# Optimization experiments

Hardware: AMD Instinct MI355X
Metric: run time of the kernel (lower is better)

The kernel has to match this reference:

```python
import jax, jax.numpy as jnp
import numpy as np

# model dims (match init_kwargs)
EMBED_DIM = 1024
NUM_HEADS = 16
HEAD_DIM = EMBED_DIM // NUM_HEADS  # 64
WS = 256           # window_size[0]*window_size[1] = 16*16
NW = 64            # number of windows
M = NW * WS        # gathered length = 16384
L = M - 1          # raw tokens (padding row appended makes M rows)
SCALE = HEAD_DIM ** -0.5


def _rope(t, cos, sin):
    # t: [M, H, d]; cos/sin: [M, d] -> broadcast over heads
    c = cos[:, None, :]
    s = sin[:, None, :]
    half = HEAD_DIM // 2
    rot = jnp.concatenate([-t[..., half:], t[..., :half]], axis=-1)
    return t * c + rot * s


def setup_inputs() -> dict:
    key = jax.random.key(0)
    ks = jax.random.split(key, 8)
    x = jax.random.normal(ks[0], (L, EMBED_DIM), jnp.float32)
    # kv_indices: permutation of all M rows (incl. padding row index L) so every
    # token lands in exactly one window slot, as the scatter-back assumes.
    kv_indices = jax.random.permutation(ks[1], M).astype(jnp.int64)
    q_indices = kv_indices            # unused in the manual (non-xformers) branch
    inv_indices = jnp.arange(L, dtype=jnp.int64)  # unused in the manual branch
    # rotary tables over gathered positions
    pos = jnp.arange(M, dtype=jnp.float32)
    inv_freq = 1.0 / (10000.0 ** (jnp.arange(0, HEAD_DIM, 2, dtype=jnp.float32) / HEAD_DIM))
    ang = pos[:, None] * inv_freq[None, :]          # [M, d/2]
    ang = jnp.concatenate([ang, ang], axis=-1)      # [M, d]
    rope_cos = jnp.cos(ang)
    rope_sin = jnp.sin(ang)
    # learned params
    qkv_w = jax.random.normal(ks[2], (3 * EMBED_DIM, EMBED_DIM), jnp.float32) * (EMBED_DIM ** -0.5)
    qkv_b = jax.random.normal(ks[3], (3 * EMBED_DIM,), jnp.float32) * 0.02
    proj_w = jax.random.normal(ks[4], (EMBED_DIM, EMBED_DIM), jnp.float32) * (EMBED_DIM ** -0.5)
    proj_b = jax.random.normal(ks[5], (EMBED_DIM,), jnp.float32) * 0.02
    padding = jnp.zeros((1, EMBED_DIM), jnp.float32)  # nn.Parameter(torch.zeros(1, D))
    return {"x": x, "qkv_w": qkv_w, "qkv_b": qkv_b, "proj_w": proj_w,
            "proj_b": proj_b, "padding": padding, "rope_cos": rope_cos,
            "rope_sin": rope_sin, "kv_indices": kv_indices,
            "q_indices": q_indices, "inv_indices": inv_indices, "ws": WS}


def reference(x, qkv_w, qkv_b, proj_w, proj_b, padding, rope_cos, rope_sin,
              kv_indices, q_indices, inv_indices, ws):
    # append padding row: [L+1, D]
    xp = jnp.concatenate([x, padding], axis=0)
    # fused qkv projection -> [M, 3, H, d]
    qkv = (xp @ qkv_w.T + qkv_b).reshape(-1, 3, NUM_HEADS, HEAD_DIM)
    q, k, v = qkv[:, 0], qkv[:, 1], qkv[:, 2]
    # manual windowed branch: gather q/k/v with kv_indices, RoPE (mode='key') on q and k
    qg = _rope(q[kv_indices], rope_cos, rope_sin)   # [M, H, d]
    kg = _rope(k[kv_indices], rope_cos, rope_sin)
    vg = v[kv_indices]
    nw = M // ws
    qw = qg.reshape(nw, ws, NUM_HEADS, HEAD_DIM)
    kw = kg.reshape(nw, ws, NUM_HEADS, HEAD_DIM)
    vw = vg.reshape(nw, ws, NUM_HEADS, HEAD_DIM)
    attn = jax.nn.softmax(SCALE * jnp.einsum('wind,wjnd->wnij', qw, kw), axis=-1)
    ow = jnp.einsum('wnij,wjnd->wind', attn, vw).reshape(M, NUM_HEADS * HEAD_DIM)
    # scatter back to original token order, drop padding row
    ori = jnp.zeros((M, EMBED_DIM), x.dtype).at[kv_indices].set(ow)
    out = ori[:L] @ proj_w.T + proj_b
    return out
```

## Files before the change

kernel.cpp:

```cpp
#include <hip/hip_runtime.h>
#include <hip/hip_bf16.h>

#define EMBED 1024
#define THREE_EMBED 3072
#define NHEAD 16
#define HDIM 64
#define MTOT 16384
#define LTOT 16383

typedef __attribute__((ext_vector_type(8))) short bf16x8;
typedef __attribute__((ext_vector_type(4))) float f32x4;

__device__ __forceinline__ unsigned short f2b(float f) {
  union { float f; unsigned u; } v; v.f = f;
  unsigned r = v.u + 0x7fffu + ((v.u >> 16) & 1u);
  return (unsigned short)(r >> 16);
}
__device__ __forceinline__ float b2f(unsigned short h) {
  union { unsigned u; float f; } v; v.u = ((unsigned)h) << 16;
  return v.f;
}

__device__ __forceinline__ void gload16(const void* g, void* l) {
  __builtin_amdgcn_global_load_lds(
      (const __attribute__((address_space(1))) void*)g,
      (__attribute__((address_space(3))) void*)l, 16, 0, 0);
}

#define BARRIER() asm volatile("s_barrier" ::: "memory")

__global__ __launch_bounds__(256) void cast_inputs(
    const float* __restrict__ x, const float* __restrict__ padding,
    const float* __restrict__ wq, const float* __restrict__ wp,
    const int* __restrict__ kvi,
    unsigned short* __restrict__ xb, unsigned short* __restrict__ wqb,
    unsigned short* __restrict__ wpb, int* __restrict__ inv, int np)
{
  const int NX = MTOT * EMBED / 8;
  const int NQ = THREE_EMBED * EMBED / 8;
  const int total = NX + NQ + np;
  int g = blockIdx.x * 256 + threadIdx.x;
  const int stride = gridDim.x * 256;
  for (; g < total + MTOT; g += stride) {
    if (g >= total) {
      int i = g - total;
      inv[kvi[i]] = i;
      continue;
    }
    const float* src;
    unsigned short* dst;
    if (g < NX) {
      size_t e = (size_t)g * 8;
      int row = (int)(e >> 10);
      src = (row < LTOT) ? (x + e) : (padding + (e - (size_t)LTOT * 1024));
      dst = xb + e;
    } else if (g < NX + NQ) {
      size_t e = (size_t)(g - NX) * 8;
      src = wq + e;
      dst = wqb + e;
    } else {
      size_t e = (size_t)(g - NX - NQ) * 8;
      src = wp + e;
      dst = wpb + e;
    }
    float4 a = *(const float4*)src;
    float4 b = *(const float4*)(src + 4);
    ushort4 u0, u1;
    u0.x = f2b(a.x); u0.y = f2b(a.y); u0.z = f2b(a.z); u0.w = f2b(a.w);
    u1.x = f2b(b.x); u1.y = f2b(b.y); u1.z = f2b(b.z); u1.w = f2b(b.w);
    *(ushort4*)dst = u0;
    *(ushort4*)(dst + 4) = u1;
  }
}

template <int EPI>
__global__ __launch_bounds__(512, 2) void gemm256(
    const unsigned short* __restrict__ A, const unsigned short* __restrict__ B,
    const float* __restrict__ bias, const int* __restrict__ idx,
    unsigned short* __restrict__ outb, float* __restrict__ outf)
{
  __shared__ __align__(16) unsigned short lds[65536];
  const int t = threadIdx.x;
  const int lane = t & 63, wid = t >> 6;
  const int l15 = lane & 15, quad = lane >> 4;
  const int wr = wid >> 2, wc = wid & 3;
  const int bm = blockIdx.x, bn = blockIdx.y;

  const int srow = wid * 8 + (lane >> 3);
  const int scol = ((lane & 7) ^ (lane >> 3)) * 8;
  const unsigned short* gA = A + (size_t)(bm * 256 + srow) * EMBED + scol;
  const unsigned short* gB = B + (size_t)(bn * 256 + srow) * EMBED + scol;

  auto stA = [&](int p, int R0, int kt) {
    const unsigned short* g = gA + (size_t)R0 * EMBED + kt * 64;
    char* d = (char*)lds + p * 32768 + R0 * 128 + wid * 1024;
    gload16(g, d);
    gload16(g + (size_t)64 * EMBED, d + 8192);
  };
  auto stB = [&](int p, int R0, int kt) {
    const unsigned short* g = gB + (size_t)R0 * EMBED + kt * 64;
    char* d = (char*)lds + 65536 + p * 32768 + R0 * 128 + wid * 1024;
    gload16(g, d);
    gload16(g + (size_t)64 * EMBED, d + 8192);
  };

  const int aOff = (wr * 128 + l15) * 64;
  const int bOff = (wc * 64 + l15) * 64;
  const int swz0 = (quad ^ (l15 & 7)) * 8;
  const int swz1 = ((quad + 4) ^ (l15 & 7)) * 8;

  f32x4 acc[8][4];
#pragma unroll
  for (int i = 0; i < 8; ++i)
#pragma unroll
    for (int j = 0; j < 4; ++j) acc[i][j] = (f32x4){0.f, 0.f, 0.f, 0.f};

  stA(0, 0, 0); stA(0, 128, 0); stB(0, 0, 0); stB(0, 128, 0);
  stB(1, 0, 1); stB(1, 128, 1);
  asm volatile("s_waitcnt vmcnt(4)" ::: "memory");
  BARRIER();

#define MFMAGRP(MB)                                                          \
  _Pragma("unroll") for (int m = 0; m < 4; ++m)                              \
      _Pragma("unroll") for (int n = 0; n < 4; ++n)                          \
          acc[(MB) + m][n] = __builtin_amdgcn_mfma_f32_16x16x32_bf16(        \
              a[m], b[n], acc[(MB) + m][n], 0, 0, 0);

#define TILE(P, KT, STA, STB, WCNT)                                          \
  {                                                                          \
    const unsigned short* Ab = lds + (P) * 16384 + aOff;                     \
    const unsigned short* Bb = lds + 32768 + (P) * 16384 + bOff;             \
    bf16x8 a[4], b[4];                                                       \
    {                                               \
      _Pragma("unroll") for (int n = 0; n < 4; ++n)                          \
          b[n] = *(const bf16x8*)(Bb + n * 1024 + swz0);                     \
      _Pragma("unroll") for (int m = 0; m < 4; ++m)                          \
          a[m] = *(const bf16x8*)(Ab + m * 1024 + swz0);                     \
      if (STA) stA((P) ^ 1, 0, (KT) + 1);                                    \
      BARRIER();                                                             \
      __builtin_amdgcn_s_setprio(1);                                         \
      MFMAGRP(0);                                                            \
      __builtin_amdgcn_s_setprio(0);                                         \
      BARRIER();                                                             \
    }                                                                        \
    {                                               \
      _Pragma("unroll") for (int m = 0; m < 4; ++m)                          \
          a[m] = *(const bf16x8*)(Ab + (4 + m) * 1024 + swz0);               \
      if (STA) stA((P) ^ 1, 128, (KT) + 1);                                  \
      BARRIER();                                                             \
      __builtin_amdgcn_s_setprio(1);                                         \
      MFMAGRP(4);                                                            \
      __builtin_amdgcn_s_setprio(0);                                         \
      BARRIER();                                                             \
    }                                                                        \
    {                                               \
      _Pragma("unroll") for (int n = 0; n < 4; ++n)                          \
          b[n] = *(const bf16x8*)(Bb + n * 1024 + swz1);                     \
      _Pragma("unroll") for (int m = 0; m < 4; ++m)                          \
          a[m] = *(const bf16x8*)(Ab + m * 1024 + swz1);                     \
      if (STB) stB((P), 0, (KT) + 2);                                        \
      BARRIER();                                                             \
      __builtin_amdgcn_s_setprio(1);                                         \
      MFMAGRP(0);                                                            \
      __builtin_amdgcn_s_setprio(0);                                         \
      BARRIER();                                                             \
    }                                                                        \
    {                                               \
      _Pragma("unroll") for (int m = 0; m < 4; ++m)                          \
          a[m] = *(const bf16x8*)(Ab + (4 + m) * 1024 + swz1);               \
      if (STB) stB((P), 128, (KT) + 2);                                      \
      BARRIER();                                                             \
      __builtin_amdgcn_s_setprio(1);                                         \
      MFMAGRP(4);                                                            \
      __builtin_amdgcn_s_setprio(0);                                         \
      if ((WCNT) == 4) asm volatile("s_waitcnt vmcnt(4)" ::: "memory");      \
      if ((WCNT) == 0) asm volatile("s_waitcnt vmcnt(0)" ::: "memory");      \
      BARRIER();                                                             \
    }                                                                        \
  }

#pragma unroll 1
  for (int t2 = 0; t2 < 7; ++t2) {
    const int kt = t2 * 2;
    TILE(0, kt, 1, 1, 4);
    TILE(1, kt + 1, 1, 1, 4);
  }
  TILE(0, 14, 1, 0, 0);
  TILE(1, 15, 0, 0, -1);
#undef TILE
#undef MFMAGRP

  float bv[4];
#pragma unroll
  for (int nt = 0; nt < 4; ++nt)
    bv[nt] = bias[bn * 256 + wc * 64 + nt * 16 + l15];
  if constexpr (EPI == 0) {
    const int hh = bn * 4 + wc;
    unsigned short* buf = outb + (size_t)hh * (MTOT * HDIM);
#pragma unroll
    for (int mt = 0; mt < 8; ++mt) {
#pragma unroll
      for (int reg = 0; reg < 4; ++reg) {
        int row = bm * 256 + wr * 128 + mt * 16 + quad * 4 + reg;
        int i = idx[row];
#pragma unroll
        for (int nt = 0; nt < 4; ++nt)
          buf[(size_t)i * HDIM + nt * 16 + l15] =
              f2b(acc[mt][nt][reg] + bv[nt]);
      }
    }
  } else {
    const int col = bn * 256 + wc * 64;
#pragma unroll
    for (int mt = 0; mt < 8; ++mt) {
#pragma unroll
      for (int reg = 0; reg < 4; ++reg) {
        int i = bm * 256 + wr * 128 + mt * 16 + quad * 4 + reg;
        int orow = idx[i];
        if (orow < LTOT) {
#pragma unroll
          for (int nt = 0; nt < 4; ++nt)
            outf[(size_t)orow * EMBED + col + nt * 16 + l15] =
                acc[mt][nt][reg] + bv[nt];
        }
      }
    }
  }
}

__global__ __launch_bounds__(256) void rope_qk(
    const float* __restrict__ rope_cos, const float* __restrict__ rope_sin,
    unsigned short* __restrict__ qkvh)
{
  int g = blockIdx.x * 256 + threadIdx.x;
  int dc = g & 3;
  int i  = (g >> 2) & (MTOT - 1);
  int hh = g >> 16;
  unsigned short* p = qkvh + ((size_t)hh * MTOT + i) * HDIM;
  bf16x8 lo = *(const bf16x8*)(p + dc * 8);
  bf16x8 hi = *(const bf16x8*)(p + 32 + dc * 8);
  const float* cp = rope_cos + (size_t)i * HDIM + dc * 8;
  const float* sp = rope_sin + (size_t)i * HDIM + dc * 8;
  float cl[8], ch[8], sl[8], sh[8];
  *(float4*)(cl)     = *(const float4*)(cp);
  *(float4*)(cl + 4) = *(const float4*)(cp + 4);
  *(float4*)(ch)     = *(const float4*)(cp + 32);
  *(float4*)(ch + 4) = *(const float4*)(cp + 36);
  *(float4*)(sl)     = *(const float4*)(sp);
  *(float4*)(sl + 4) = *(const float4*)(sp + 4);
  *(float4*)(sh)     = *(const float4*)(sp + 32);
  *(float4*)(sh + 4) = *(const float4*)(sp + 36);
  const float sc = (hh < 16) ? 0.125f : 1.0f;
  bf16x8 olo, ohi;
#pragma unroll
  for (int j = 0; j < 8; ++j) {
    float a = b2f((unsigned short)lo[j]);
    float b = b2f((unsigned short)hi[j]);
    olo[j] = (short)f2b((a * cl[j] - b * sl[j]) * sc);
    ohi[j] = (short)f2b((b * ch[j] + a * sh[j]) * sc);
  }
  *(bf16x8*)(p + dc * 8) = olo;
  *(bf16x8*)(p + 32 + dc * 8) = ohi;
}

__global__ __launch_bounds__(256) void cast_w(
    const float* __restrict__ w, unsigned short* __restrict__ wb)
{
  int g = blockIdx.x * 256 + threadIdx.x;
  size_t e = (size_t)g * 8;
  float4 a = *(const float4*)(w + e);
  float4 b = *(const float4*)(w + e + 4);
  ushort4 u0, u1;
  u0.x = f2b(a.x); u0.y = f2b(a.y); u0.z = f2b(a.z); u0.w = f2b(a.w);
  u1.x = f2b(b.x); u1.y = f2b(b.y); u1.z = f2b(b.z); u1.w = f2b(b.w);
  *(ushort4*)(wb + e) = u0;
  *(ushort4*)(wb + e + 4) = u1;
}

__global__ __launch_bounds__(256, 2) void attn(
    const unsigned short* __restrict__ qkvh,
    unsigned short* __restrict__ ow)
{
  __shared__ __align__(16) unsigned short sK[2][128 * 64];
  __shared__ __align__(16) unsigned short sV[2][64 * 128];
  __shared__ __align__(16) unsigned short sP[4][16 * 40];

  const int t = threadIdx.x;
  const int lane = t & 63, wid = t >> 6;
  const int l15 = lane & 15, quad = lane >> 4;
  const int wwin = blockIdx.x >> 4;
  const int h = blockIdx.x & 15;

  const unsigned short* Qh = qkvh + (size_t)h * (MTOT * HDIM);
  const unsigned short* Kh = qkvh + (size_t)(16 + h) * (MTOT * HDIM);
  const unsigned short* Vh = qkvh + (size_t)(32 + h) * (MTOT * HDIM);

  const int l3 = lane >> 3, l7 = lane & 7;
  const unsigned short* ksrc =
      Kh + (size_t)(wwin * 256 + wid * 32 + l3) * HDIM + (l7 ^ l3) * 8;
  auto stageK = [&](int buf, int half) {
#pragma unroll
    for (int p = 0; p < 4; ++p)
      gload16(ksrc + (size_t)(half * 128 + p * 8) * HDIM,
              (char*)&sK[buf][(wid * 32 + p * 8) * 64]);
  };

  const int vkey = t >> 1, vhx = t & 1;
  const unsigned short* vsrc =
      Vh + (size_t)(wwin * 256 + vkey) * HDIM + vhx * 32;
  auto writeV = [&](int buf, bf16x8* vr) {
    int kc3 = vkey >> 3, k7 = vkey & 7;
#pragma unroll
    for (int c = 0; c < 4; ++c)
#pragma unroll
      for (int j = 0; j < 8; ++j) {
        int d = vhx * 32 + c * 8 + j;
        sV[buf][d * 128 + ((kc3 ^ (d & 7)) * 8) + k7] =
            (unsigned short)vr[c][j];
      }
  };

  f32x4 accO[4][4];
  float mrow[4][4], lrow[4][4];
#pragma unroll
  for (int qt = 0; qt < 4; ++qt) {
#pragma unroll
    for (int nt = 0; nt < 4; ++nt) accO[qt][nt] = (f32x4){0.f, 0.f, 0.f, 0.f};
#pragma unroll
    for (int reg = 0; reg < 4; ++reg) { mrow[qt][reg] = -1e30f; lrow[qt][reg] = 0.f; }
  }

  stageK(0, 0);
  bf16x8 vr0[4], vr1[4];
#pragma unroll
  for (int c = 0; c < 4; ++c) vr0[c] = *(const bf16x8*)(vsrc + c * 8);
  bf16x8 qa[4][2];
#pragma unroll
  for (int qt = 0; qt < 4; ++qt) {
    int i = wwin * 256 + wid * 64 + qt * 16 + l15;
    const unsigned short* qp = Qh + (size_t)i * HDIM;
    qa[qt][0] = *(const bf16x8*)(qp + quad * 8);
    qa[qt][1] = *(const bf16x8*)(qp + 32 + quad * 8);
  }
  asm volatile("s_waitcnt vmcnt(0)" ::: "memory");
  writeV(0, vr0);
  stageK(1, 1);
#pragma unroll
  for (int c = 0; c < 4; ++c)
    vr1[c] = *(const bf16x8*)(vsrc + (size_t)128 * HDIM + c * 8);
  __syncthreads();

  auto compute = [&](const unsigned short* sKb, const unsigned short* sVb) {
#pragma unroll
    for (int qt = 0; qt < 4; ++qt) {
      f32x4 accS[8];
#pragma unroll
      for (int nt = 0; nt < 8; ++nt) accS[nt] = (f32x4){0.f, 0.f, 0.f, 0.f};
#pragma unroll
      for (int ks = 0; ks < 2; ++ks) {
#pragma unroll
        for (int nt = 0; nt < 8; ++nt) {
          int key = nt * 16 + l15;
          bf16x8 bk = *(const bf16x8*)(
              sKb + key * 64 + (((ks * 4 + quad) ^ (key & 7)) * 8));
          accS[nt] = __builtin_amdgcn_mfma_f32_16x16x32_bf16(
              qa[qt][ks], bk, accS[nt], 0, 0, 0);
        }
      }
#pragma unroll
      for (int reg = 0; reg < 4; ++reg) {
        float mx = accS[0][reg];
#pragma unroll
        for (int nt = 1; nt < 8; ++nt) mx = fmaxf(mx, accS[nt][reg]);
#pragma unroll
        for (int off = 1; off < 16; off <<= 1)
          mx = fmaxf(mx, __shfl_xor(mx, off, 64));
        float mold = mrow[qt][reg];
        float mnew = fmaxf(mold, mx);
        float alpha = __expf(mold - mnew);
        mrow[qt][reg] = mnew;
        float ls = 0.f;
#pragma unroll
        for (int nt = 0; nt < 8; ++nt) {
          float p = __expf(accS[nt][reg] - mnew);
          accS[nt][reg] = p;
          ls += p;
        }
#pragma unroll
        for (int off = 1; off < 16; off <<= 1) ls += __shfl_xor(ls, off, 64);
        lrow[qt][reg] = lrow[qt][reg] * alpha + ls;
#pragma unroll
        for (int nt = 0; nt < 4; ++nt) accO[qt][nt][reg] *= alpha;
      }
#pragma unroll
      for (int kc = 0; kc < 4; ++kc) {
#pragma unroll
        for (int nt2 = 0; nt2 < 2; ++nt2) {
#pragma unroll
          for (int reg = 0; reg < 4; ++reg) {
            sP[wid][(quad * 4 + reg) * 40 + nt2 * 16 + l15] =
                f2b(accS[kc * 2 + nt2][reg]);
          }
        }
        bf16x8 pa = *(const bf16x8*)(&sP[wid][l15 * 40 + quad * 8]);
#pragma unroll
        for (int nt = 0; nt < 4; ++nt) {
          int d = nt * 16 + l15;
          bf16x8 bv = *(const bf16x8*)(
              sVb + d * 128 + (((kc * 4 + quad) ^ (d & 7)) * 8));
          accO[qt][nt] = __builtin_amdgcn_mfma_f32_16x16x32_bf16(
              pa, bv, accO[qt][nt], 0, 0, 0);
        }
      }
    }
  };

  compute(&sK[0][0], &sV[0][0]);
  asm volatile("s_waitcnt vmcnt(0)" ::: "memory");
  __syncthreads();
  writeV(1, vr1);
  __syncthreads();
  compute(&sK[1][0], &sV[1][0]);

  __syncthreads();
  unsigned short* scr = &sK[0][0] + wid * 2048;
  const int rlane = lane >> 3;
  const int clane = (lane & 7) * 8;
#pragma unroll
  for (int qt = 0; qt < 4; ++qt) {
#pragma unroll
    for (int reg = 0; reg < 4; ++reg) {
      float invl = 1.0f / lrow[qt][reg];
      int r = quad * 4 + reg;
#pragma unroll
      for (int nt = 0; nt < 4; ++nt)
        scr[r * 72 + nt * 16 + l15] = f2b(accO[qt][nt][reg] * invl);
    }
#pragma unroll
    for (int rr = 0; rr < 2; ++rr) {
      int row = rr * 8 + rlane;
      bf16x8 vv = *(const bf16x8*)(scr + row * 72 + clane);
      int i = wwin * 256 + wid * 64 + qt * 16 + row;
      *(bf16x8*)(ow + (size_t)i * EMBED + h * HDIM + clane) = vv;
    }
  }
}

extern "C" void kernel_launch(void* const* d_in, const int* in_sizes, int n_in,
                              void* d_out, int out_size, void* d_ws, size_t ws_size,
                              hipStream_t stream) {
  const float* x        = (const float*)d_in[0];
  const float* qkv_w    = (const float*)d_in[1];
  const float* qkv_b    = (const float*)d_in[2];
  const float* proj_w   = (const float*)d_in[3];
  const float* proj_b   = (const float*)d_in[4];
  const float* padding  = (const float*)d_in[5];
  const float* rope_cos = (const float*)d_in[6];
  const float* rope_sin = (const float*)d_in[7];
  const int*   kvi      = (const int*)d_in[8];

  const size_t QKVH_B = (size_t)MTOT * THREE_EMBED * 2;
  const size_t R_B    = (size_t)MTOT * EMBED * 2;
  const size_t W_B    = (size_t)EMBED * EMBED * 2;
  unsigned short* qkvh = (unsigned short*)d_ws;
  unsigned short* R    = (unsigned short*)((char*)d_ws + QKVH_B);
  unsigned short* xb = R;
  unsigned short* ow = R;
  unsigned short* wqb = (unsigned short*)d_out;
  const bool roomy = ws_size >= QKVH_B + R_B + W_B;
  unsigned short* wpb = roomy
      ? (unsigned short*)((char*)d_ws + QKVH_B + R_B)
      : qkvh;
  int* inv = (int*)((char*)d_out + (size_t)LTOT * EMBED * 4 - (size_t)MTOT * 4);
  float* out = (float*)d_out;

  cast_inputs<<<4096, 256, 0, stream>>>(
      x, padding, qkv_w, roomy ? proj_w : nullptr, kvi, xb, wqb, wpb, inv,
      roomy ? (EMBED * EMBED / 8) : 0);
  gemm256<0><<<dim3(64, 12), 512, 0, stream>>>(xb, wqb, qkv_b, inv, qkvh,
                                               nullptr);
  rope_qk<<<8192, 256, 0, stream>>>(rope_cos, rope_sin, qkvh);
  attn<<<dim3(64 * 16), 256, 0, stream>>>(qkvh, ow);
  if (!roomy) cast_w<<<512, 256, 0, stream>>>(proj_w, wpb);
  gemm256<1><<<dim3(64, 4), 512, 0, stream>>>(ow, wpb, proj_b, kvi, nullptr,
                                              out);
}
```

Before: 366.3 us.

## Process two heads per attention block with cross-head K/V prefetch pipeline

Each attention workgroup now handles two heads of one window instead of one, halving the grid to 512 blocks. K/V staging for the second head is issued while the first head is still computing, so the load latency of the next head overlaps with MFMA work. The epilogue scratch moves from sK into an enlarged sP buffer so it does not collide with in-flight K staging. The trade-off is more registers (two Q fragments held at once) and fewer blocks, which may lower occupancy and parallelism on a 256-CU device.

```diff
diff --git a/kernel.cpp b/kernel.cpp
--- a/kernel.cpp
+++ b/kernel.cpp
@@ -28,6 +28,8 @@
 }
 
 #define BARRIER() asm volatile("s_barrier" ::: "memory")
+#define VMCNT(N) asm volatile("s_waitcnt vmcnt(" #N ")" ::: "memory")
+#define LGKM0()  asm volatile("s_waitcnt lgkmcnt(0)" ::: "memory")
 
 __global__ __launch_bounds__(256) void cast_inputs(
     const float* __restrict__ x, const float* __restrict__ padding,
@@ -283,31 +285,37 @@
 {
   __shared__ __align__(16) unsigned short sK[2][128 * 64];
   __shared__ __align__(16) unsigned short sV[2][64 * 128];
-  __shared__ __align__(16) unsigned short sP[4][16 * 40];
+  __shared__ __align__(16) unsigned short sP[4][16 * 72];
 
   const int t = threadIdx.x;
   const int lane = t & 63, wid = t >> 6;
   const int l15 = lane & 15, quad = lane >> 4;
-  const int wwin = blockIdx.x >> 4;
-  const int h = blockIdx.x & 15;
-
-  const unsigned short* Qh = qkvh + (size_t)h * (MTOT * HDIM);
-  const unsigned short* Kh = qkvh + (size_t)(16 + h) * (MTOT * HDIM);
-  const unsigned short* Vh = qkvh + (size_t)(32 + h) * (MTOT * HDIM);
+  const int wwin = blockIdx.x >> 3;
+  const int hp = blockIdx.x & 7;
+  const int h0 = hp * 2, h1 = hp * 2 + 1;
+
+  const unsigned short* Qb = qkvh;
+  const unsigned short* Kb = qkvh + (size_t)16 * (MTOT * HDIM);
+  const unsigned short* Vb = qkvh + (size_t)32 * (MTOT * HDIM);
 
   const int l3 = lane >> 3, l7 = lane & 7;
-  const unsigned short* ksrc =
-      Kh + (size_t)(wwin * 256 + wid * 32 + l3) * HDIM + (l7 ^ l3) * 8;
-  auto stageK = [&](int buf, int half) {
+  auto stageK = [&](int buf, int h, int half) {
+    const unsigned short* src = Kb + (size_t)h * (MTOT * HDIM) +
+        (size_t)(wwin * 256 + half * 128 + wid * 32 + l3) * HDIM +
+        (l7 ^ l3) * 8;
 #pragma unroll
     for (int p = 0; p < 4; ++p)
-      gload16(ksrc + (size_t)(half * 128 + p * 8) * HDIM,
+      gload16(src + (size_t)(p * 8) * HDIM,
               (char*)&sK[buf][(wid * 32 + p * 8) * 64]);
   };
 
   const int vkey = t >> 1, vhx = t & 1;
-  const unsigned short* vsrc =
-      Vh + (size_t)(wwin * 256 + vkey) * HDIM + vhx * 32;
+  auto loadV = [&](int h, int half, bf16x8* vr) {
+    const unsigned short* src = Vb + (size_t)h * (MTOT * HDIM) +
+        (size_t)(wwin * 256 + half * 128 + vkey) * HDIM + vhx * 32;
+#pragma unroll
+    for (int c = 0; c < 4; ++c) vr[c] = *(const bf16x8*)(src + c * 8);
+  };
   auto writeV = [&](int buf, bf16x8* vr) {
     int kc3 = vkey >> 3, k7 = vkey & 7;
 #pragma unroll
@@ -320,37 +328,32 @@
       }
   };
 
+  auto loadQ = [&](int h, bf16x8 (&qa)[4][2]) {
+#pragma unroll
+    for (int qt = 0; qt < 4; ++qt) {
+      int i = wwin * 256 + wid * 64 + qt * 16 + l15;
+      const unsigned short* qp = Qb + (size_t)h * (MTOT * HDIM) +
+                                 (size_t)i * HDIM;
+      qa[qt][0] = *(const bf16x8*)(qp + quad * 8);
+      qa[qt][1] = *(const bf16x8*)(qp + 32 + quad * 8);
+    }
+  };
+
   f32x4 accO[4][4];
   float mrow[4][4], lrow[4][4];
-#pragma unroll
-  for (int qt = 0; qt < 4; ++qt) {
-#pragma unroll
-    for (int nt = 0; nt < 4; ++nt) accO[qt][nt] = (f32x4){0.f, 0.f, 0.f, 0.f};
-#pragma unroll
-    for (int reg = 0; reg < 4; ++reg) { mrow[qt][reg] = -1e30f; lrow[qt][reg] = 0.f; }
-  }
-
-  stageK(0, 0);
-  bf16x8 vr0[4], vr1[4];
-#pragma unroll
-  for (int c = 0; c < 4; ++c) vr0[c] = *(const bf16x8*)(vsrc + c * 8);
-  bf16x8 qa[4][2];
-#pragma unroll
-  for (int qt = 0; qt < 4; ++qt) {
-    int i = wwin * 256 + wid * 64 + qt * 16 + l15;
-    const unsigned short* qp = Qh + (size_t)i * HDIM;
-    qa[qt][0] = *(const bf16x8*)(qp + quad * 8);
-    qa[qt][1] = *(const bf16x8*)(qp + 32 + quad * 8);
-  }
-  asm volatile("s_waitcnt vmcnt(0)" ::: "memory");
-  writeV(0, vr0);
-  stageK(1, 1);
-#pragma unroll
-  for (int c = 0; c < 4; ++c)
-    vr1[c] = *(const bf16x8*)(vsrc + (size_t)128 * HDIM + c * 8);
-  __syncthreads();
-
-  auto compute = [&](const unsigned short* sKb, const unsigned short* sVb) {
+  auto resetAcc = [&]() {
+#pragma unroll
+    for (int qt = 0; qt < 4; ++qt) {
+#pragma unroll
+      for (int nt = 0; nt < 4; ++nt) accO[qt][nt] = (f32x4){0.f, 0.f, 0.f, 0.f};
+#pragma unroll
+      for (int reg = 0; reg < 4; ++reg) { mrow[qt][reg] = -1e30f; lrow[qt][reg] = 0.f; }
+    }
+  };
+  resetAcc();
+
+  auto compute = [&](const unsigned short* sKb, const unsigned short* sVb,
+                     const bf16x8 (&qa)[4][2]) {
 #pragma unroll
     for (int qt = 0; qt < 4; ++qt) {
       f32x4 accS[8];
@@ -415,35 +418,73 @@
     }
   };
 
-  compute(&sK[0][0], &sV[0][0]);
-  asm volatile("s_waitcnt vmcnt(0)" ::: "memory");
-  __syncthreads();
-  writeV(1, vr1);
-  __syncthreads();
-  compute(&sK[1][0], &sV[1][0]);
-
-  __syncthreads();
-  unsigned short* scr = &sK[0][0] + wid * 2048;
   const int rlane = lane >> 3;
   const int clane = (lane & 7) * 8;
-#pragma unroll
-  for (int qt = 0; qt < 4; ++qt) {
-#pragma unroll
-    for (int reg = 0; reg < 4; ++reg) {
-      float invl = 1.0f / lrow[qt][reg];
-      int r = quad * 4 + reg;
-#pragma unroll
-      for (int nt = 0; nt < 4; ++nt)
-        scr[r * 72 + nt * 16 + l15] = f2b(accO[qt][nt][reg] * invl);
-    }
-#pragma unroll
-    for (int rr = 0; rr < 2; ++rr) {
-      int row = rr * 8 + rlane;
-      bf16x8 vv = *(const bf16x8*)(scr + row * 72 + clane);
-      int i = wwin * 256 + wid * 64 + qt * 16 + row;
-      *(bf16x8*)(ow + (size_t)i * EMBED + h * HDIM + clane) = vv;
-    }
-  }
+  auto epilogue = [&](int h) {
+    unsigned short* scr = &sP[wid][0];
+#pragma unroll
+    for (int qt = 0; qt < 4; ++qt) {
+#pragma unroll
+      for (int reg = 0; reg < 4; ++reg) {
+        float invl = 1.0f / lrow[qt][reg];
+        int r = quad * 4 + reg;
+#pragma unroll
+        for (int nt = 0; nt < 4; ++nt)
+          scr[r * 72 + nt * 16 + l15] = f2b(accO[qt][nt][reg] * invl);
+      }
+#pragma unroll
+      for (int rr = 0; rr < 2; ++rr) {
+        int row = rr * 8 + rlane;
+        bf16x8 vv = *(const bf16x8*)(scr + row * 72 + clane);
+        int i = wwin * 256 + wid * 64 + qt * 16 + row;
+        *(bf16x8*)(ow + (size_t)i * EMBED + h * HDIM + clane) = vv;
+      }
+    }
+  };
+
+  bf16x8 vr0[4], vr1[4];
+  bf16x8 qa0[4][2], qa1[4][2];
+
+  stageK(0, h0, 0);
+  loadV(h0, 0, vr0);
+  loadQ(h0, qa0);
+  loadQ(h1, qa1);
+  VMCNT(0);
+  writeV(0, vr0);
+  stageK(1, h0, 1);
+  loadV(h0, 1, vr1);
+  LGKM0();
+  BARRIER();
+
+  compute(&sK[0][0], &sV[0][0], qa0);
+  VMCNT(0);
+  BARRIER();
+  writeV(1, vr1);
+  stageK(0, h1, 0);
+  loadV(h1, 0, vr0);
+  LGKM0();
+  BARRIER();
+
+  compute(&sK[1][0], &sV[1][0], qa0);
+  VMCNT(0);
+  BARRIER();
+  writeV(0, vr0);
+  stageK(1, h1, 1);
+  loadV(h1, 1, vr1);
+  epilogue(h0);
+  resetAcc();
+  LGKM0();
+  BARRIER();
+
+  compute(&sK[0][0], &sV[0][0], qa1);
+  VMCNT(8);
+  BARRIER();
+  writeV(1, vr1);
+  LGKM0();
+  BARRIER();
+
+  compute(&sK[1][0], &sV[1][0], qa1);
+  epilogue(h1);
 }
 
 extern "C" void kernel_launch(void* const* d_in, const int* in_sizes, int n_in,
@@ -480,7 +521,7 @@
   gemm256<0><<<dim3(64, 12), 512, 0, stream>>>(xb, wqb, qkv_b, inv, qkvh,
                                                nullptr);
   rope_qk<<<8192, 256, 0, stream>>>(rope_cos, rope_sin, qkvh);
-  attn<<<dim3(64 * 16), 256, 0, stream>>>(qkvh, ow);
+  attn<<<dim3(64 * 8), 256, 0, stream>>>(qkvh, ow);
   if (!roomy) cast_w<<<512, 256, 0, stream>>>(proj_w, wpb);
   gemm256<1><<<dim3(64, 4), 512, 0, stream>>>(ow, wpb, proj_b, kvi, nullptr,
                                               out);
```

Measured after the change: 413.7 us. 1.13x slower.
